# Kernel tuning notes

Hardware: AMD Instinct MI355X
Metric: run time of the kernel (lower is better)

Reference implementation:

```python
import jax, jax.numpy as jnp
import numpy as np

HALF = 32          # (input_dim-1)//2
HIDDEN = 128
OUT_DIM = 10
B, T, C = 256, 512, 65


def setup_inputs() -> dict:
    key = jax.random.key(0)
    ks = jax.random.split(key, 20)
    s = 0.05
    gin = HALF + HIDDEN
    inp = {
        "times": jnp.arange(T, dtype=jnp.float32),
        "coeff_a": jax.random.normal(ks[0], (B, T - 1, C), jnp.float32),
        "coeff_b": jax.random.normal(ks[1], (B, T - 1, C), jnp.float32),
        "coeff_two_c": jax.random.normal(ks[2], (B, T - 1, C), jnp.float32),
        "coeff_three_d": jax.random.normal(ks[3], (B, T - 1, C), jnp.float32),
        "final_index": jax.random.randint(ks[4], (B,), 0, T),
        "Wr": jax.random.normal(ks[5], (gin, HIDDEN), jnp.float32) * s,
        "br": jnp.zeros((HIDDEN,), jnp.float32),
        "Wz": jax.random.normal(ks[6], (gin, HIDDEN), jnp.float32) * s,
        "bz": jnp.zeros((HIDDEN,), jnp.float32),
        "Wxn": jax.random.normal(ks[7], (HALF, HIDDEN), jnp.float32) * s,
        "bxn": jnp.zeros((HIDDEN,), jnp.float32),
        "Whn": jax.random.normal(ks[8], (HIDDEN, HIDDEN), jnp.float32) * s,
        "bhn": jnp.zeros((HIDDEN,), jnp.float32),
        "W_ode": jax.random.normal(ks[9], (HIDDEN, HIDDEN), jnp.float32) * s,
        "b_ode": jnp.zeros((HIDDEN,), jnp.float32),
        "W_lin": jax.random.normal(ks[10], (HIDDEN, OUT_DIM), jnp.float32) * s,
        "b_lin": jnp.zeros((OUT_DIM,), jnp.float32),
    }
    return inp


def _forward(times, coeff_a, coeff_b, coeff_two_c, coeff_three_d, final_index,
             Wr, br, Wz, bz, Wxn, bxn, Whn, bhn, W_ode, b_ode, W_lin, b_lin):
    maxlen = coeff_b.shape[-2] - 1

    def eval_spline(t):
        idx = jnp.clip(jnp.sum(t > times) - 1, 0, maxlen)
        fr = t - times[idx]
        inner = 0.5 * coeff_two_c[:, idx, :] + coeff_three_d[:, idx, :] * (fr / 3.0)
        inner = coeff_b[:, idx, :] + inner * fr
        return coeff_a[:, idx, :] + inner * fr  # [B, C]

    X = jax.vmap(eval_spline, out_axes=1)(times)  # [B, T, C]
    # difference the observation-indicator channels over time; make channel 0 a time delta
    X = X.at[:, 1:, 1:1 + HALF].add(-X[:, :-1, 1:1 + HALF])
    X = X.at[:, 0, 0].add(-times[0])
    X = X.at[:, 1:, 0].add(-times[:-1])

    nbatch = X.shape[0]

    def gru(x, h):
        comb = jnp.concatenate([x, h], axis=1)
        r = jax.nn.sigmoid(comb @ Wr + br)
        z = jax.nn.sigmoid(comb @ Wz + bz)
        n = jnp.tanh(x @ Wxn + bxn + (h @ Whn + bhn) * r)
        return (1.0 - z) * n + z * h

    def f_ode(h):
        return jnp.tanh(h @ W_ode + b_ode)

    def evolve(h, td):
        # single RK4 step from 0 to td
        k1 = f_ode(h)
        k2 = f_ode(h + 0.5 * td * k1)
        k3 = f_ode(h + 0.5 * td * k2)
        k4 = f_ode(h + td * k3)
        return h + (td / 6.0) * (k1 + 2.0 * k2 + 2.0 * k3 + k4)

    def step(h, dt, Xi):
        obs = jnp.max(Xi[:, 1:1 + HALF], axis=1) > 0.5
        Xp = Xi[:, 1 + HALF:].at[:, 0].add(dt)
        new_h = gru(Xp, h)

        def take(hd):
            h0, dt0 = hd
            return (jnp.where(obs[:, None], new_h, h0),
                    dt0 + jnp.where(obs, 0.0, Xi[:, 0]))

        return jax.lax.cond(jnp.any(obs), take, lambda hd: hd, (h, dt))

    z0 = jnp.zeros((nbatch, HIDDEN), X.dtype)
    dt0 = jnp.zeros((nbatch,), X.dtype)
    h0, dt0 = step(z0, dt0, X[:, 0])

    time_diffs = times[1:] - times[:-1]
    Xs = jnp.moveaxis(X[:, 1:], 1, 0)  # [T-1, B, C]

    def scan_body(carry, inp):
        h, dt = carry
        td, Xi = inp
        h = evolve(h, td)
        h, dt = step(h, dt, Xi)
        return (h, dt), h

    _, hs_rest = jax.lax.scan(scan_body, (h0, dt0), (time_diffs, Xs))
    out = jnp.concatenate([h0[:, None], jnp.moveaxis(hs_rest, 0, 1)], axis=1)  # [B, T, H]
    final = out[jnp.arange(nbatch), final_index]  # [B, H]
    return final @ W_lin + b_lin


def reference(times, coeff_a, coeff_b, coeff_two_c, coeff_three_d, final_index,
              Wr, br, Wz, bz, Wxn, bxn, Whn, bhn, W_ode, b_ode, W_lin, b_lin):
    return _forward(times, coeff_a, coeff_b, coeff_two_c, coeff_three_d, final_index,
                    Wr, br, Wz, bz, Wxn, bxn, Whn, bhn, W_ode, b_ode, W_lin, b_lin)
```

## Files before the change

kernel.cpp:

```cpp
#include <hip/hip_runtime.h>
#include <string.h>

#define TT 512
#define BB 256
#define CC 65
#define HALFC 32
#define HID 128
#define ODIM 10

typedef _Float16 half2_t __attribute__((ext_vector_type(2)));
typedef _Float16 half8_t __attribute__((ext_vector_type(8)));

__device__ __forceinline__ float ftanh(float x) {
  float u = __builtin_amdgcn_exp2f(x * -2.885390082f);
  return fmaf(2.f, __builtin_amdgcn_rcpf(1.f + u), -1.f);
}
__device__ __forceinline__ float fsig(float x) {
  float u = __builtin_amdgcn_exp2f(x * -1.442695041f);
  return __builtin_amdgcn_rcpf(1.f + u);
}

__device__ __forceinline__ half2_t h2cvt(float a, float b) {
  auto r = __builtin_amdgcn_cvt_pkrtz(a, b);
  half2_t o;
  memcpy(&o, &r, sizeof(o));
  return o;
}

__device__ __forceinline__ float fdot2h(half2_t a, half2_t b, float c) {
  return __builtin_amdgcn_fdot2(a, b, c, false);
}

template <int CTRL>
__device__ __forceinline__ float dpp_add(float x) {
  return x + __int_as_float(__builtin_amdgcn_update_dpp(
      0, __float_as_int(x), CTRL, 0xF, 0xF, true));
}
__device__ __forceinline__ float red4(float x) {
  x = dpp_add<0x101>(x);
  x = dpp_add<0x102>(x);
  return x;
}

__device__ __forceinline__ void block_sync_lds() {
  asm volatile("s_waitcnt lgkmcnt(0)" ::: "memory");
  __builtin_amdgcn_s_barrier();
  asm volatile("" ::: "memory");
}
__device__ __forceinline__ void vm_wait0() {
  asm volatile("s_waitcnt vmcnt(0)" ::: "memory");
}

__global__ void prep0(const float* __restrict__ times, float4* __restrict__ si,
                      int* __restrict__ anyobs) {
  __shared__ float ts[TT];
  int t = threadIdx.x;
  ts[t] = times[t];
  __syncthreads();
  float tv = ts[t];
  int cnt = 0;
  for (int jj = 0; jj < TT; ++jj) cnt += (tv > ts[jj]) ? 1 : 0;
  int idx = cnt - 1;
  idx = min(max(idx, 0), TT - 2);
  float4 o;
  o.x = __int_as_float(idx);
  o.y = tv - ts[idx];
  o.z = (t == 0) ? 0.f : (tv - ts[t - 1]);
  o.w = (t == 0) ? ts[0] : ts[t - 1];
  si[t] = o;
  anyobs[t] = 0;
}

__global__ void prep_obs(const float* __restrict__ ca, const float* __restrict__ cb,
                         const float* __restrict__ cc2, const float* __restrict__ cd,
                         const float4* __restrict__ si, int* __restrict__ anyobs,
                         unsigned char* __restrict__ obs) {
  int grp = blockIdx.x * (blockDim.x >> 5) + (threadIdx.x >> 5);
  int lane = threadIdx.x & 31;
  int t = grp & (TT - 1);
  int b = grp / TT;
  int ch = 1 + lane;
  float4 s = si[t];
  int idx = __float_as_int(s.x);
  float fr = s.y;
  size_t base = ((size_t)b * (TT - 1) + idx) * CC + ch;
  float f3 = fr / 3.f;
  float v = ca[base] + (cb[base] + (0.5f * cc2[base] + cd[base] * f3) * fr) * fr;
  float D = v;
  if (t >= 1) {
    float4 sp = si[t - 1];
    int idxp = __float_as_int(sp.x);
    float frp = sp.y;
    size_t basep = ((size_t)b * (TT - 1) + idxp) * CC + ch;
    float f3p = frp / 3.f;
    float vp = ca[basep] + (cb[basep] + (0.5f * cc2[basep] + cd[basep] * f3p) * frp) * frp;
    D = v - vp;
  }
  float m = D;
  #pragma unroll
  for (int off = 16; off >= 1; off >>= 1) m = fmaxf(m, __shfl_xor(m, off));
  if (lane == 0) {
    unsigned char o = (m > 0.5f) ? (unsigned char)1 : (unsigned char)0;
    obs[(size_t)b * TT + t] = o;
    if (o) atomicOr(&anyobs[t], 1);
  }
}

__launch_bounds__(256, 1)
__global__ void ode_main(
    const float* __restrict__ ca, const float* __restrict__ cb,
    const float* __restrict__ cc2, const float* __restrict__ cd,
    const int* __restrict__ final_index,
    const float* __restrict__ Wr, const float* __restrict__ br,
    const float* __restrict__ Wz, const float* __restrict__ bz,
    const float* __restrict__ Wxn, const float* __restrict__ bxn,
    const float* __restrict__ Whn, const float* __restrict__ bhn,
    const float* __restrict__ Wode, const float* __restrict__ bode,
    const float* __restrict__ Wlin, const float* __restrict__ blin,
    const float4* __restrict__ si, const int* __restrict__ anyobs,
    const unsigned char* __restrict__ obsArr,
    float* __restrict__ out)
{
  __shared__ alignas(16) half2_t hS2[HID / 2];
  __shared__ alignas(16) half2_t vA2[HID / 2];
  __shared__ alignas(16) half2_t vB2[HID / 2];
  __shared__ alignas(16) _Float16 xh[HALFC];
  __shared__ float xs0f;
  __shared__ alignas(16) float4 siL[TT];
  __shared__ unsigned char flagL[TT];

  const int tid = threadIdx.x;
  const int b = blockIdx.x;
  const int lane = tid & 63;
  const int wv = tid >> 6;
  const int p = lane >> 2;
  const int kk = lane & 3;
  const int s = wv * 16 + p;
  const int j0 = 2 * s;
  const int wbyte = 4 * s;

  half2_t wodeH[32], whnH[32], wrhH[32], wzhH[32];
  #pragma unroll
  for (int i = 0; i < 16; ++i) {
    const int r0 = 32 * kk + 2 * i, r1 = r0 + 1;
    float2 q0, q1;
    q0 = *(const float2*)&Wode[r0 * HID + j0];
    q1 = *(const float2*)&Wode[r1 * HID + j0];
    wodeH[2*i] = h2cvt(q0.x, q1.x); wodeH[2*i+1] = h2cvt(q0.y, q1.y);
    q0 = *(const float2*)&Whn[r0 * HID + j0];
    q1 = *(const float2*)&Whn[r1 * HID + j0];
    whnH[2*i] = h2cvt(q0.x, q1.x); whnH[2*i+1] = h2cvt(q0.y, q1.y);
    q0 = *(const float2*)&Wr[(HALFC + r0) * HID + j0];
    q1 = *(const float2*)&Wr[(HALFC + r1) * HID + j0];
    wrhH[2*i] = h2cvt(q0.x, q1.x); wrhH[2*i+1] = h2cvt(q0.y, q1.y);
    q0 = *(const float2*)&Wz[(HALFC + r0) * HID + j0];
    q1 = *(const float2*)&Wz[(HALFC + r1) * HID + j0];
    wzhH[2*i] = h2cvt(q0.x, q1.x); wzhH[2*i+1] = h2cvt(q0.y, q1.y);
  }
  half2_t wrxH[8], wzxH[8], wxnH[8];
  #pragma unroll
  for (int i = 0; i < 4; ++i) {
    const int c0 = 8 * kk + 2 * i, c1 = c0 + 1;
    float2 q0, q1;
    q0 = *(const float2*)&Wr[c0 * HID + j0];
    q1 = *(const float2*)&Wr[c1 * HID + j0];
    wrxH[i] = h2cvt(q0.x, q1.x); wrxH[4+i] = h2cvt(q0.y, q1.y);
    q0 = *(const float2*)&Wz[c0 * HID + j0];
    q1 = *(const float2*)&Wz[c1 * HID + j0];
    wzxH[i] = h2cvt(q0.x, q1.x); wzxH[4+i] = h2cvt(q0.y, q1.y);
    q0 = *(const float2*)&Wxn[c0 * HID + j0];
    q1 = *(const float2*)&Wxn[c1 * HID + j0];
    wxnH[i] = h2cvt(q0.x, q1.x); wxnH[4+i] = h2cvt(q0.y, q1.y);
  }
  float wr0a = 0.f, wr0b = 0.f, wz0a = 0.f, wz0b = 0.f, wx0a = 0.f, wx0b = 0.f;
  if (kk == 0) {
    wrxH[0][0] = (_Float16)0.f; wrxH[4][0] = (_Float16)0.f;
    wzxH[0][0] = (_Float16)0.f; wzxH[4][0] = (_Float16)0.f;
    wxnH[0][0] = (_Float16)0.f; wxnH[4][0] = (_Float16)0.f;
    wr0a = Wr[j0];  wr0b = Wr[j0 + 1];
    wz0a = Wz[j0];  wz0b = Wz[j0 + 1];
    wx0a = Wxn[j0]; wx0b = Wxn[j0 + 1];
  }
  float bo0, bo1, bh0, bh1, br0, br1, bz0, bz1, bx0, bx1;
  { float2 q;
    q = *(const float2*)&bode[j0]; bo0 = q.x; bo1 = q.y;
    q = *(const float2*)&bhn [j0]; bh0 = q.x; bh1 = q.y;
    q = *(const float2*)&br  [j0]; br0 = q.x; br1 = q.y;
    q = *(const float2*)&bz  [j0]; bz0 = q.x; bz1 = q.y;
    q = *(const float2*)&bxn [j0]; bx0 = q.x; bx1 = q.y;
  }
  const int fidx = final_index[b];

  #pragma unroll
  for (int it = 0; it < 2; ++it) {
    const int tt = tid + it * 256;
    siL[tt] = si[tt];
    const int ao = anyobs[tt];
    const unsigned char o = obsArr[(size_t)b * TT + tt];
    flagL[tt] = (unsigned char)((ao ? 1 : 0) | (o ? 2 : 0));
  }
  if (tid < HID / 2) {
    const half2_t z2 = {(_Float16)0.f, (_Float16)0.f};
    hS2[tid] = z2; vA2[tid] = z2; vB2[tid] = z2;
  }
  if (tid < HALFC) xh[tid] = (_Float16)0.f;
  if (tid == 0) xs0f = 0.f;
  float hj0 = 0.f, hj1 = 0.f;
  float dtv = 0.f;
  block_sync_lds();

  auto mv = [&](const half2_t* __restrict__ buf, const half2_t (&w)[32],
                float& o0, float& o1) {
    half2_t v2[16];
    #pragma unroll
    for (int q = 0; q < 4; ++q) {
      const half8_t x8 = *(const half8_t*)((const char*)buf + 64 * kk + 16 * q);
      v2[4*q+0] = __builtin_shufflevector(x8, x8, 0, 1);
      v2[4*q+1] = __builtin_shufflevector(x8, x8, 2, 3);
      v2[4*q+2] = __builtin_shufflevector(x8, x8, 4, 5);
      v2[4*q+3] = __builtin_shufflevector(x8, x8, 6, 7);
    }
    float a0 = 0.f, a1 = 0.f, b0 = 0.f, b1 = 0.f;
    #pragma unroll
    for (int i = 0; i < 8; ++i) {
      a0 = fdot2h(v2[i],     w[2*i],       a0);
      a1 = fdot2h(v2[i],     w[2*i+1],     a1);
      b0 = fdot2h(v2[8 + i], w[2*(8+i)],   b0);
      b1 = fdot2h(v2[8 + i], w[2*(8+i)+1], b1);
    }
    o0 = red4(a0 + b0);
    o1 = red4(a1 + b1);
  };

  float4 sv4 = siL[0];
  int flg = flagL[0];

  for (int t = 0; ; ++t) {
    const int sidx = __float_as_int(sv4.x);
    const float fr = sv4.y, td = sv4.z, tsub = sv4.w;
    const bool apply = (flg & 1) && (flg & 2);

    const int xch = wv * 8 + lane;
    const bool xlane = (lane < 8);
    float xa = 0.f, xb = 0.f, xc = 0.f, xd = 0.f;
    float ya = 0.f, yb = 0.f, yc = 0.f, yd = 0.f;
    if (xlane) {
      const size_t base = ((size_t)b * (TT - 1) + sidx) * CC;
      const int ch = 33 + xch;
      xa = ca[base + ch]; xb = cb[base + ch]; xc = cc2[base + ch]; xd = cd[base + ch];
      if (tid == 0) { ya = ca[base]; yb = cb[base]; yc = cc2[base]; yd = cd[base]; }
    }

    if (t > 0) {
      const float htd = 0.5f * td;
      float p0, p1, k0, k1, ks0, ks1;
      mv(hS2, wodeH, p0, p1);
      k0 = ftanh(p0 + bo0); k1 = ftanh(p1 + bo1);
      ks0 = k0; ks1 = k1;
      if (kk == 0)
        *(half2_t*)((char*)vA2 + wbyte) =
            h2cvt(fmaf(htd, k0, hj0), fmaf(htd, k1, hj1));
      block_sync_lds();
      mv(vA2, wodeH, p0, p1);
      k0 = ftanh(p0 + bo0); k1 = ftanh(p1 + bo1);
      ks0 = fmaf(2.f, k0, ks0); ks1 = fmaf(2.f, k1, ks1);
      if (kk == 0)
        *(half2_t*)((char*)vB2 + wbyte) =
            h2cvt(fmaf(htd, k0, hj0), fmaf(htd, k1, hj1));
      block_sync_lds();
      mv(vB2, wodeH, p0, p1);
      k0 = ftanh(p0 + bo0); k1 = ftanh(p1 + bo1);
      ks0 = fmaf(2.f, k0, ks0); ks1 = fmaf(2.f, k1, ks1);
      if (kk == 0)
        *(half2_t*)((char*)vA2 + wbyte) =
            h2cvt(fmaf(td, k0, hj0), fmaf(td, k1, hj1));
      block_sync_lds();
      mv(vA2, wodeH, p0, p1);
      k0 = ftanh(p0 + bo0); k1 = ftanh(p1 + bo1);
      ks0 += k0; ks1 += k1;
      hj0 = fmaf(td * (1.f / 6.f), ks0, hj0);
      hj1 = fmaf(td * (1.f / 6.f), ks1, hj1);
      if (kk == 0)
        *(half2_t*)((char*)vB2 + wbyte) = h2cvt(hj0, hj1);
    }

    float xdelta = 0.f;
    vm_wait0();
    if (xlane) {
      const float f3 = fr * (1.f / 3.f);
      float sv = xa + (xb + (0.5f * xc + xd * f3) * fr) * fr;
      if (tid == 0) {
        const float s0 = ya + (yb + (0.5f * yc + yd * f3) * fr) * fr;
        xdelta = s0 - tsub;
        sv += dtv;
        xs0f = sv;
      }
      xh[xch] = (_Float16)sv;
    }
    block_sync_lds();

    {
      half2_t v2[16];
      #pragma unroll
      for (int q = 0; q < 4; ++q) {
        const half8_t x8 = *(const half8_t*)((const char*)vB2 + 64 * kk + 16 * q);
        v2[4*q+0] = __builtin_shufflevector(x8, x8, 0, 1);
        v2[4*q+1] = __builtin_shufflevector(x8, x8, 2, 3);
        v2[4*q+2] = __builtin_shufflevector(x8, x8, 4, 5);
        v2[4*q+3] = __builtin_shufflevector(x8, x8, 6, 7);
      }
      float rp0 = 0.f, rp1 = 0.f, zp0 = 0.f, zp1 = 0.f, gp0 = 0.f, gp1 = 0.f;
      #pragma unroll
      for (int i = 0; i < 16; ++i) {
        rp0 = fdot2h(v2[i], wrhH[2*i],   rp0);
        rp1 = fdot2h(v2[i], wrhH[2*i+1], rp1);
        zp0 = fdot2h(v2[i], wzhH[2*i],   zp0);
        zp1 = fdot2h(v2[i], wzhH[2*i+1], zp1);
        gp0 = fdot2h(v2[i], whnH[2*i],   gp0);
        gp1 = fdot2h(v2[i], whnH[2*i+1], gp1);
      }
      float xp0 = 0.f, xp1 = 0.f;
      {
        const half8_t x8 = *(const half8_t*)((const char*)xh + 16 * kk);
        half2_t xv2[4];
        xv2[0] = __builtin_shufflevector(x8, x8, 0, 1);
        xv2[1] = __builtin_shufflevector(x8, x8, 2, 3);
        xv2[2] = __builtin_shufflevector(x8, x8, 4, 5);
        xv2[3] = __builtin_shufflevector(x8, x8, 6, 7);
        #pragma unroll
        for (int i = 0; i < 4; ++i) {
          rp0 = fdot2h(xv2[i], wrxH[i],   rp0);
          rp1 = fdot2h(xv2[i], wrxH[4+i], rp1);
          zp0 = fdot2h(xv2[i], wzxH[i],   zp0);
          zp1 = fdot2h(xv2[i], wzxH[4+i], zp1);
          xp0 = fdot2h(xv2[i], wxnH[i],   xp0);
          xp1 = fdot2h(xv2[i], wxnH[4+i], xp1);
        }
      }
      if (kk == 0) {
        const float x0 = xs0f;
        rp0 = fmaf(x0, wr0a, rp0); rp1 = fmaf(x0, wr0b, rp1);
        zp0 = fmaf(x0, wz0a, zp0); zp1 = fmaf(x0, wz0b, zp1);
        xp0 = fmaf(x0, wx0a, xp0); xp1 = fmaf(x0, wx0b, xp1);
      }
      rp0 = red4(rp0); rp1 = red4(rp1);
      zp0 = red4(zp0); zp1 = red4(zp1);
      gp0 = red4(gp0); gp1 = red4(gp1);
      xp0 = red4(xp0); xp1 = red4(xp1);
      const float r0 = fsig(rp0 + br0), r1 = fsig(rp1 + br1);
      const float z0 = fsig(zp0 + bz0), z1 = fsig(zp1 + bz1);
      const float n0 = ftanh(xp0 + bx0 + (gp0 + bh0) * r0);
      const float n1 = ftanh(xp1 + bx1 + (gp1 + bh1) * r1);
      const float h0n = fmaf(z0, hj0 - n0, n0);
      const float h1n = fmaf(z1, hj1 - n1, n1);
      hj0 = apply ? h0n : hj0;
      hj1 = apply ? h1n : hj1;
      if (kk == 0)
        *(half2_t*)((char*)hS2 + wbyte) = h2cvt(hj0, hj1);
    }
    if (tid == 0 && (flg & 1) && !(flg & 2)) dtv += xdelta;

    if (t == fidx) break;
    const int tn = t + 1;
    sv4 = siL[tn];
    flg = flagL[tn];
    block_sync_lds();
  }

  block_sync_lds();
  if (tid < ODIM) {
    float acc = blin[tid];
    const _Float16* hf = (const _Float16*)hS2;
    #pragma unroll 8
    for (int q = 0; q < HID; ++q) {
      const float hv = (float)hf[q];
      acc = fmaf(hv, Wlin[q * ODIM + tid], acc);
    }
    out[b * ODIM + tid] = acc;
  }
}

extern "C" void kernel_launch(void* const* d_in, const int* in_sizes, int n_in,
                              void* d_out, int out_size, void* d_ws, size_t ws_size,
                              hipStream_t stream) {
  const float* times = (const float*)d_in[0];
  const float* ca   = (const float*)d_in[1];
  const float* cb   = (const float*)d_in[2];
  const float* cc2  = (const float*)d_in[3];
  const float* cd   = (const float*)d_in[4];
  const int*   fidx = (const int*)d_in[5];
  const float* Wr   = (const float*)d_in[6];
  const float* br   = (const float*)d_in[7];
  const float* Wz   = (const float*)d_in[8];
  const float* bz   = (const float*)d_in[9];
  const float* Wxn  = (const float*)d_in[10];
  const float* bxn  = (const float*)d_in[11];
  const float* Whn  = (const float*)d_in[12];
  const float* bhn  = (const float*)d_in[13];
  const float* Wode = (const float*)d_in[14];
  const float* bode = (const float*)d_in[15];
  const float* Wlin = (const float*)d_in[16];
  const float* blin = (const float*)d_in[17];
  float* out = (float*)d_out;

  char* ws = (char*)d_ws;
  float4* si = (float4*)ws;
  int* anyobs = (int*)(ws + TT * 16);
  unsigned char* obs = (unsigned char*)(ws + TT * 16 + TT * 4);

  prep0<<<1, TT, 0, stream>>>(times, si, anyobs);
  prep_obs<<<(BB * TT) / 8, 256, 0, stream>>>(ca, cb, cc2, cd, si, anyobs, obs);
  ode_main<<<BB, 256, 0, stream>>>(ca, cb, cc2, cd, fidx, Wr, br, Wz, bz,
                                   Wxn, bxn, Whn, bhn, Wode, bode, Wlin, blin,
                                   si, anyobs, obs, out);
}
```

Baseline: 956.8 us.

## Prefetch next-step spline coefficients and overlap input projection with ODE stages

The global loads of spline coefficients for the next time step are issued one iteration early, so their latency overlaps with the current step's ODE and GRU work. The input-side GRU projections are moved between the RK4 matrix-vector stages, where they overlap with the ODE computation. The GRU update, and the barrier that follows it, are now skipped entirely on steps where the flag says no GRU is needed. This trims serial latency on the recurrence but changes the apply condition and leaves the shared hidden buffer un-refreshed on skipped steps, which risks correctness.

```diff
diff --git a/kernel.cpp b/kernel.cpp
--- a/kernel.cpp
+++ b/kernel.cpp
@@ -232,24 +232,50 @@
     o1 = red4(a1 + b1);
   };
 
+  const int xch = wv * 8 + lane;
+  const bool xlane = (lane < 8);
+
   float4 sv4 = siL[0];
   int flg = flagL[0];
 
+  float xa = 0.f, xb = 0.f, xc = 0.f, xd = 0.f;
+  float ya = 0.f, yb = 0.f, yc = 0.f, yd = 0.f;
+  if (xlane) {
+    const size_t base = ((size_t)b * (TT - 1) + __float_as_int(sv4.x)) * CC;
+    const int ch = 33 + xch;
+    xa = ca[base + ch]; xb = cb[base + ch]; xc = cc2[base + ch]; xd = cd[base + ch];
+    if (tid == 0) { ya = ca[base]; yb = cb[base]; yc = cc2[base]; yd = cd[base]; }
+  }
+
   for (int t = 0; ; ++t) {
-    const int sidx = __float_as_int(sv4.x);
     const float fr = sv4.y, td = sv4.z, tsub = sv4.w;
-    const bool apply = (flg & 1) && (flg & 2);
-
-    const int xch = wv * 8 + lane;
-    const bool xlane = (lane < 8);
-    float xa = 0.f, xb = 0.f, xc = 0.f, xd = 0.f;
-    float ya = 0.f, yb = 0.f, yc = 0.f, yd = 0.f;
+    const bool doGru = (flg & 2) != 0;
+
+    float xdelta = 0.f;
+    vm_wait0();
     if (xlane) {
-      const size_t base = ((size_t)b * (TT - 1) + sidx) * CC;
+      const float f3 = fr * (1.f / 3.f);
+      float sv = xa + (xb + (0.5f * xc + xd * f3) * fr) * fr;
+      if (tid == 0) {
+        const float s0 = ya + (yb + (0.5f * yc + yd * f3) * fr) * fr;
+        xdelta = s0 - tsub;
+        sv += dtv;
+        xs0f = sv;
+      }
+      xh[xch] = (_Float16)sv;
+    }
+
+    const int tn = (t < TT - 1) ? t + 1 : t;
+    const float4 sv4N = siL[tn];
+    const int flgN = flagL[tn];
+    if (xlane) {
+      const size_t base = ((size_t)b * (TT - 1) + __float_as_int(sv4N.x)) * CC;
       const int ch = 33 + xch;
       xa = ca[base + ch]; xb = cb[base + ch]; xc = cc2[base + ch]; xd = cd[base + ch];
       if (tid == 0) { ya = ca[base]; yb = cb[base]; yc = cc2[base]; yd = cd[base]; }
     }
+
+    float rxp0 = 0.f, rxp1 = 0.f, zxp0 = 0.f, zxp1 = 0.f, xxp0 = 0.f, xxp1 = 0.f;
 
     if (t > 0) {
       const float htd = 0.5f * td;
@@ -261,6 +287,29 @@
         *(half2_t*)((char*)vA2 + wbyte) =
             h2cvt(fmaf(htd, k0, hj0), fmaf(htd, k1, hj1));
       block_sync_lds();
+      if (doGru) {
+        const half8_t x8 = *(const half8_t*)((const char*)xh + 16 * kk);
+        half2_t xv2[4];
+        xv2[0] = __builtin_shufflevector(x8, x8, 0, 1);
+        xv2[1] = __builtin_shufflevector(x8, x8, 2, 3);
+        xv2[2] = __builtin_shufflevector(x8, x8, 4, 5);
+        xv2[3] = __builtin_shufflevector(x8, x8, 6, 7);
+        #pragma unroll
+        for (int i = 0; i < 4; ++i) {
+          rxp0 = fdot2h(xv2[i], wrxH[i],   rxp0);
+          rxp1 = fdot2h(xv2[i], wrxH[4+i], rxp1);
+          zxp0 = fdot2h(xv2[i], wzxH[i],   zxp0);
+          zxp1 = fdot2h(xv2[i], wzxH[4+i], zxp1);
+          xxp0 = fdot2h(xv2[i], wxnH[i],   xxp0);
+          xxp1 = fdot2h(xv2[i], wxnH[4+i], xxp1);
+        }
+        if (kk == 0) {
+          const float x0 = xs0f;
+          rxp0 = fmaf(x0, wr0a, rxp0); rxp1 = fmaf(x0, wr0b, rxp1);
+          zxp0 = fmaf(x0, wz0a, zxp0); zxp1 = fmaf(x0, wz0b, zxp1);
+          xxp0 = fmaf(x0, wx0a, xxp0); xxp1 = fmaf(x0, wx0b, xxp1);
+        }
+      }
       mv(vA2, wodeH, p0, p1);
       k0 = ftanh(p0 + bo0); k1 = ftanh(p1 + bo1);
       ks0 = fmaf(2.f, k0, ks0); ks1 = fmaf(2.f, k1, ks1);
@@ -282,24 +331,35 @@
       hj1 = fmaf(td * (1.f / 6.f), ks1, hj1);
       if (kk == 0)
         *(half2_t*)((char*)vB2 + wbyte) = h2cvt(hj0, hj1);
-    }
-
-    float xdelta = 0.f;
-    vm_wait0();
-    if (xlane) {
-      const float f3 = fr * (1.f / 3.f);
-      float sv = xa + (xb + (0.5f * xc + xd * f3) * fr) * fr;
-      if (tid == 0) {
-        const float s0 = ya + (yb + (0.5f * yc + yd * f3) * fr) * fr;
-        xdelta = s0 - tsub;
-        sv += dtv;
-        xs0f = sv;
+      block_sync_lds();
+    } else {
+      block_sync_lds();
+      if (doGru) {
+        const half8_t x8 = *(const half8_t*)((const char*)xh + 16 * kk);
+        half2_t xv2[4];
+        xv2[0] = __builtin_shufflevector(x8, x8, 0, 1);
+        xv2[1] = __builtin_shufflevector(x8, x8, 2, 3);
+        xv2[2] = __builtin_shufflevector(x8, x8, 4, 5);
+        xv2[3] = __builtin_shufflevector(x8, x8, 6, 7);
+        #pragma unroll
+        for (int i = 0; i < 4; ++i) {
+          rxp0 = fdot2h(xv2[i], wrxH[i],   rxp0);
+          rxp1 = fdot2h(xv2[i], wrxH[4+i], rxp1);
+          zxp0 = fdot2h(xv2[i], wzxH[i],   zxp0);
+          zxp1 = fdot2h(xv2[i], wzxH[4+i], zxp1);
+          xxp0 = fdot2h(xv2[i], wxnH[i],   xxp0);
+          xxp1 = fdot2h(xv2[i], wxnH[4+i], xxp1);
+        }
+        if (kk == 0) {
+          const float x0 = xs0f;
+          rxp0 = fmaf(x0, wr0a, rxp0); rxp1 = fmaf(x0, wr0b, rxp1);
+          zxp0 = fmaf(x0, wz0a, zxp0); zxp1 = fmaf(x0, wz0b, zxp1);
+          xxp0 = fmaf(x0, wx0a, xxp0); xxp1 = fmaf(x0, wx0b, xxp1);
+        }
       }
-      xh[xch] = (_Float16)sv;
-    }
-    block_sync_lds();
-
-    {
+    }
+
+    if (doGru) {
       half2_t v2[16];
       #pragma unroll
       for (int q = 0; q < 4; ++q) {
@@ -309,7 +369,8 @@
         v2[4*q+2] = __builtin_shufflevector(x8, x8, 4, 5);
         v2[4*q+3] = __builtin_shufflevector(x8, x8, 6, 7);
       }
-      float rp0 = 0.f, rp1 = 0.f, zp0 = 0.f, zp1 = 0.f, gp0 = 0.f, gp1 = 0.f;
+      float rp0 = rxp0, rp1 = rxp1, zp0 = zxp0, zp1 = zxp1;
+      float gp0 = 0.f, gp1 = 0.f, xp0 = xxp0, xp1 = xxp1;
       #pragma unroll
       for (int i = 0; i < 16; ++i) {
         rp0 = fdot2h(v2[i], wrhH[2*i],   rp0);
@@ -319,30 +380,6 @@
         gp0 = fdot2h(v2[i], whnH[2*i],   gp0);
         gp1 = fdot2h(v2[i], whnH[2*i+1], gp1);
       }
-      float xp0 = 0.f, xp1 = 0.f;
-      {
-        const half8_t x8 = *(const half8_t*)((const char*)xh + 16 * kk);
-        half2_t xv2[4];
-        xv2[0] = __builtin_shufflevector(x8, x8, 0, 1);
-        xv2[1] = __builtin_shufflevector(x8, x8, 2, 3);
-        xv2[2] = __builtin_shufflevector(x8, x8, 4, 5);
-        xv2[3] = __builtin_shufflevector(x8, x8, 6, 7);
-        #pragma unroll
-        for (int i = 0; i < 4; ++i) {
-          rp0 = fdot2h(xv2[i], wrxH[i],   rp0);
-          rp1 = fdot2h(xv2[i], wrxH[4+i], rp1);
-          zp0 = fdot2h(xv2[i], wzxH[i],   zp0);
-          zp1 = fdot2h(xv2[i], wzxH[4+i], zp1);
-          xp0 = fdot2h(xv2[i], wxnH[i],   xp0);
-          xp1 = fdot2h(xv2[i], wxnH[4+i], xp1);
-        }
-      }
-      if (kk == 0) {
-        const float x0 = xs0f;
-        rp0 = fmaf(x0, wr0a, rp0); rp1 = fmaf(x0, wr0b, rp1);
-        zp0 = fmaf(x0, wz0a, zp0); zp1 = fmaf(x0, wz0b, zp1);
-        xp0 = fmaf(x0, wx0a, xp0); xp1 = fmaf(x0, wx0b, xp1);
-      }
       rp0 = red4(rp0); rp1 = red4(rp1);
       zp0 = red4(zp0); zp1 = red4(zp1);
       gp0 = red4(gp0); gp1 = red4(gp1);
@@ -351,20 +388,18 @@
       const float z0 = fsig(zp0 + bz0), z1 = fsig(zp1 + bz1);
       const float n0 = ftanh(xp0 + bx0 + (gp0 + bh0) * r0);
       const float n1 = ftanh(xp1 + bx1 + (gp1 + bh1) * r1);
-      const float h0n = fmaf(z0, hj0 - n0, n0);
-      const float h1n = fmaf(z1, hj1 - n1, n1);
-      hj0 = apply ? h0n : hj0;
-      hj1 = apply ? h1n : hj1;
+      hj0 = fmaf(z0, hj0 - n0, n0);
+      hj1 = fmaf(z1, hj1 - n1, n1);
       if (kk == 0)
         *(half2_t*)((char*)hS2 + wbyte) = h2cvt(hj0, hj1);
-    }
-    if (tid == 0 && (flg & 1) && !(flg & 2)) dtv += xdelta;
+    } else {
+      if (tid == 0 && (flg & 1)) dtv += xdelta;
+    }
 
     if (t == fidx) break;
-    const int tn = t + 1;
-    sv4 = siL[tn];
-    flg = flagL[tn];
-    block_sync_lds();
+    sv4 = sv4N;
+    flg = flgN;
+    if (doGru) block_sync_lds();
   }
 
   block_sync_lds();
```

New measurement: 904.9 us, median of 2. 1.06x faster.
